# Performance work log

Hardware: AMD Instinct MI355X
Metric: run time of the kernel (lower is better)

Reference implementation:

```python
import jax, jax.numpy as jnp
import numpy as np

POOL = 14  # pool_size from __init__


def setup_inputs() -> dict:
    key = jax.random.key(0)
    k1, k2, k3, k4 = jax.random.split(key, 4)
    B, H, W, C, N = 2, 128, 128, 256, 512
    features = jax.random.normal(k1, (B, H, W, C), dtype=jnp.float32)
    # roi layout per original code: [y1, x1, y2, x2]; crop = features[img, x1:x2, y1:y2, :]
    y1 = jax.random.randint(k2, (B, N, 1), 0, H - 16)
    x1 = jax.random.randint(k3, (B, N, 1), 0, W - 16)
    hw = jax.random.randint(k4, (B, N, 2), 8, 16)  # box sizes in [8,16)
    roi = jnp.concatenate([y1, x1, y1 + hw[..., :1], x1 + hw[..., 1:]], axis=-1).astype(jnp.int32)
    return {"features": features, "roi": roi}


def _legacy_resize_axis(start, end, pool):
    """Legacy TF1 bilinear resize (align_corners=False): local src coord = i * (size/pool).
    Returns global low/high integer indices and interpolation fractions, shapes [R, pool]."""
    size = (end - start).astype(jnp.float32)  # [R]
    local = jnp.arange(pool, dtype=jnp.float32)[None, :] * size[:, None] / pool  # [R,P]
    i0 = jnp.floor(local).astype(jnp.int32)
    i1 = jnp.minimum(i0 + 1, (end - start - 1)[:, None])  # clamp inside the crop
    frac = local - i0.astype(jnp.float32)
    return start[:, None] + i0, start[:, None] + i1, frac


def reference(features, roi):
    B, H, W, C = features.shape
    N = roi.shape[1]
    pool = POOL
    roi = roi.reshape(-1, 4)  # [R,4] rows of (y1, x1, y2, x2), R = B*N
    img = jnp.repeat(jnp.arange(B, dtype=jnp.int32), N)  # image index per ROI, [R]
    y1, x1, y2, x2 = roi[:, 0], roi[:, 1], roi[:, 2], roi[:, 3]
    # Original slices rows with x1:x2 and cols with y1:y2; crop+resize == direct
    # bilinear sampling in the full map at global coords start + i*size/pool.
    r0, r1, fr = _legacy_resize_axis(x1, x2, pool)  # rows,   [R,P]
    c0, c1, fc = _legacy_resize_axis(y1, y2, pool)  # cols,   [R,P]

    def gather(r, c):
        # [R,P,P,C] fused gather over all ROIs at once (replaces tf.scan)
        return features[img[:, None, None], r[:, :, None], c[:, None, :], :]

    fr = fr[:, :, None, None]
    fc = fc[:, None, :, None]
    top = gather(r0, c0) * (1.0 - fc) + gather(r0, c1) * fc
    bot = gather(r1, c0) * (1.0 - fc) + gather(r1, c1) * fc
    return top * (1.0 - fr) + bot * fr  # [B*N, pool, pool, C]
```

## Files before the change

kernel.cpp:

```cpp
#include <hip/hip_runtime.h>


typedef float f32x4 __attribute__((ext_vector_type(4)));

#define NROI 1024
#define WAVES_TOTAL (NROI * 14)
#define THREADS 256
#define NBLK (WAVES_TOTAL / 4)

__global__ __launch_bounds__(THREADS) void rpn_pool_kernel(
    const float* __restrict__ feat,
    const int*   __restrict__ roi,
    float*       __restrict__ out)
{
    const int lane = threadIdx.x & 63;
    const int wv   = threadIdx.x >> 6;

    const int d   = blockIdx.x;
    const int blk = (d & 7) * (NBLK / 8) + (d >> 3);
    const int W   = blk * 4 + wv;
    const int q   = W / 14;
    const int i   = W - q * 14;
    const int b   = q >> 9;

    const int4 rr = ((const int4*)roi)[q];
    const int y1 = rr.x, x1 = rr.y, y2 = rr.z, x2 = rr.w;
    const int sR = x2 - x1;
    const int sC = y2 - y1;

    const int pr  = i * sR;
    const int ir0 = pr / 14;
    const float fr  = (float)(pr - ir0 * 14) * (1.0f / 14.0f);
    const float wr1 = 1.0f - fr;
    const int r0 = ir0;
    const int r1 = min(ir0 + 1, sR - 1);

    const size_t SB4 = (size_t)128 * 128 * 64;
    const size_t SR4 = (size_t)128 * 64;
    const f32x4* base = (const f32x4*)feat + (size_t)b * SB4
                        + (size_t)x1 * SR4 + (size_t)y1 * 64 + lane;
    const f32x4* rowA = base + (size_t)r0 * SR4;
    const f32x4* rowB = base + (size_t)r1 * SR4;

    int cA = 0, cB = min(1, sC - 1);
    f32x4 a0 = rowA[0];
    f32x4 a1 = rowA[(size_t)cB * 64];
    f32x4 b0 = rowB[0];
    f32x4 b1 = rowB[(size_t)cB * 64];

    f32x4* outp = (f32x4*)out + ((size_t)q * 196 + (size_t)i * 14) * 64 + lane;

    for (int j = 0; j < 14; ++j) {
        const int pc = j * sC;
        const float fc = (float)(pc - cA * 14) * (1.0f / 14.0f);

        int nA = cA, nB = cB;
        f32x4 p0, p1;
        bool adv = false;
        if (j < 13) {
            nA = ((j + 1) * sC) / 14;
            nB = min(nA + 1, sC - 1);
            if (nB > cB) {
                p0 = rowA[(size_t)nB * 64];
                p1 = rowB[(size_t)nB * 64];
                adv = true;
            }
        }

        f32x4 o = (a0 * (1.0f - fc) + a1 * fc) * wr1 + (b0 * (1.0f - fc) + b1 * fc) * fr;

        f32x4* p = outp + (size_t)j * 64;
        asm volatile("global_store_dwordx4 %0, %1, off sc0 sc1 nt"
                     :: "v"(p), "v"(o) : "memory");

        if (nA > cA) { a0 = a1; b0 = b1; }
        if (adv)     { a1 = p0; b1 = p1; }
        cA = nA; cB = nB;
    }
}

extern "C" void kernel_launch(void* const* d_in, const int* in_sizes, int n_in,
                              void* d_out, int out_size, void* d_ws, size_t ws_size,
                              hipStream_t stream) {
    const float* feat = (const float*)d_in[0];
    const int*   roi  = (const int*)d_in[1];
    float* out = (float*)d_out;

    rpn_pool_kernel<<<NBLK, THREADS, 0, stream>>>(feat, roi, out);
}
```

Before: 50.39 us.

## Reorder ROI processing by spatial Morton buckets to improve feature cache locality

Adds a single-block pre-kernel that buckets the ROIs by image and a Morton code of their coarse top-left position, then writes a permutation. The pooling kernel processes ROIs in this permuted order so that spatially nearby ROIs are handled by neighbouring blocks and share cached feature rows. In exchange it adds an extra kernel launch with a serial O(N) rank loop per thread, plus one indirection load per wave.

New measurement: 63.85 us. +26.7%, slower.

```diff
diff --git a/kernel.cpp b/kernel.cpp
--- a/kernel.cpp
+++ b/kernel.cpp
@@ -7,10 +7,46 @@
 #define WAVES_TOTAL (NROI * 14)
 #define THREADS 256
 #define NBLK (WAVES_TOTAL / 4)
+#define NBUCKET 128
+
+__device__ __forceinline__ unsigned spread3(unsigned v) {
+    v &= 7u;
+    return (v & 1u) | ((v & 2u) << 1) | ((v & 4u) << 2);
+}
+
+__global__ __launch_bounds__(1024) void roi_bucket_kernel(
+    const int* __restrict__ roi, int* __restrict__ perm)
+{
+    __shared__ short bkt[NROI];
+    __shared__ int cnt[NBUCKET];
+    __shared__ int basearr[NBUCKET];
+    const int t = threadIdx.x;
+    if (t < NBUCKET) cnt[t] = 0;
+    __syncthreads();
+
+    const int4 rr = ((const int4*)roi)[t];
+    const int b = t >> 9;
+    const unsigned m = spread3((unsigned)rr.y >> 4) | (spread3((unsigned)rr.x >> 4) << 1);
+    const int bucket = (b << 6) | (int)m;
+    bkt[t] = (short)bucket;
+    atomicAdd(&cnt[bucket], 1);
+    __syncthreads();
+
+    if (t == 0) {
+        int acc = 0;
+        for (int k = 0; k < NBUCKET; ++k) { basearr[k] = acc; acc += cnt[k]; }
+    }
+    __syncthreads();
+
+    int rank = 0;
+    for (int k = 0; k < t; ++k) rank += (bkt[k] == (short)bucket);
+    perm[basearr[bucket] + rank] = t;
+}
 
 __global__ __launch_bounds__(THREADS) void rpn_pool_kernel(
     const float* __restrict__ feat,
     const int*   __restrict__ roi,
+    const int*   __restrict__ perm,
     float*       __restrict__ out)
 {
     const int lane = threadIdx.x & 63;
@@ -19,8 +55,9 @@
     const int d   = blockIdx.x;
     const int blk = (d & 7) * (NBLK / 8) + (d >> 3);
     const int W   = blk * 4 + wv;
-    const int q   = W / 14;
-    const int i   = W - q * 14;
+    const int g   = W / 14;
+    const int i   = W - g * 14;
+    const int q   = perm[g];
     const int b   = q >> 9;
 
     const int4 rr = ((const int4*)roi)[q];
@@ -85,6 +122,8 @@
     const float* feat = (const float*)d_in[0];
     const int*   roi  = (const int*)d_in[1];
     float* out = (float*)d_out;
+    int*   perm = (int*)d_ws;
 
-    rpn_pool_kernel<<<NBLK, THREADS, 0, stream>>>(feat, roi, out);
+    roi_bucket_kernel<<<1, 1024, 0, stream>>>(roi, perm);
+    rpn_pool_kernel<<<NBLK, THREADS, 0, stream>>>(feat, roi, perm, out);
 }
```
